# Optimization experiments

Hardware: AMD Instinct MI355X
Metric: run time of the kernel (lower is better)

Reference implementation:

```python
import jax, jax.numpy as jnp
import numpy as np

N_HEAD = 8
FACTOR = 5


def setup_inputs() -> dict:
    key = jax.random.key(0)
    ks = jax.random.split(key, 6)
    B, L, D = 2, 2048, 512
    sample_k = FACTOR * int(np.ceil(np.log(L)))  # 40
    std = float(np.sqrt(2.0 / (D + D)))
    x = jax.random.normal(ks[0], (B, L, D), jnp.float32)
    Wq = jax.random.normal(ks[1], (D, D), jnp.float32) * std
    Wk = jax.random.normal(ks[2], (D, D), jnp.float32) * std
    Wv = jax.random.normal(ks[3], (D, D), jnp.float32) * std
    bq = jnp.zeros((D,), jnp.float32)
    bk = jnp.zeros((D,), jnp.float32)
    bv = jnp.zeros((D,), jnp.float32)
    index_sample = jax.random.randint(ks[4], (L, sample_k), 0, L, dtype=jnp.int64)
    return {"x": x, "Wq": Wq, "bq": bq, "Wk": Wk, "bk": bk, "Wv": Wv, "bv": bv,
            "index_sample": index_sample}


def reference(x, Wq, bq, Wk, bk, Wv, bv, index_sample):
    B, L, D = x.shape
    H = N_HEAD
    dk = D // H
    u = min(FACTOR * int(np.ceil(np.log(L))), L)  # n_top == sample_k here

    def proj(W, b):
        # nn.Linear: x @ W.T + b, then split heads -> [B, H, L, dk]
        return (x @ W.T + b).reshape(B, L, H, dk).transpose(0, 2, 1, 3)

    q, k, v = proj(Wq, bq), proj(Wk, bk), proj(Wv, bv)

    # --- _prob_QK: sampled QK scores for query sparsity measure ---
    # K_sample[b,h,l,s,:] = k[b,h, index_sample[l,s], :]
    K_sample = k[:, :, index_sample]                      # [B,H,L,S,dk]
    Q_K_sample = jnp.einsum('bhld,bhlsd->bhls', q, K_sample)  # [B,H,L,S]
    M = Q_K_sample.max(-1) - Q_K_sample.sum(-1) / L       # sparsity measure [B,H,L]
    M_top = jax.lax.top_k(M, u)[1]                        # [B,H,u] top-query indices

    Q_reduce = jnp.take_along_axis(q, M_top[..., None], axis=2)  # [B,H,u,dk]
    scale = 1.0 / np.sqrt(dk)
    scores = jnp.einsum('bhud,bhld->bhul', Q_reduce, k) * scale  # [B,H,u,L]

    # --- initial context: causal cumulative sum of V (mask_flag=True) ---
    context = jnp.cumsum(v, axis=2)                       # [B,H,L,dk]

    # --- update context at the selected query rows ---
    attn = jax.nn.softmax(scores, axis=-1)                # [B,H,u,L]
    upd = jnp.einsum('bhul,bhld->bhud', attn, v)          # [B,H,u,dk]
    bidx = jnp.arange(B)[:, None, None]
    hidx = jnp.arange(H)[None, :, None]
    context = context.at[bidx, hidx, M_top].set(upd)

    attns = jnp.full((B, H, L, L), 1.0 / L, dtype=attn.dtype)
    attns = attns.at[bidx, hidx, M_top].set(attn)

    # NOTE: original reshapes [B,H,L,dk] -> [B,L,H*dk] WITHOUT transposing; keep faithful.
    return context.reshape(B, L, -1), attns
```

## Files before the change

### kernel.cpp

```cpp
#include <hip/hip_runtime.h>
#include <math.h>

#define BB 2
#define LL 2048
#define DD 512
#define HH 8
#define DK 64
#define SK 40
#define UU 40
#define BH (BB*HH)

typedef __attribute__((ext_vector_type(8))) __bf16 bf16x8;
typedef __attribute__((ext_vector_type(4))) float f32x4;

__device__ inline ushort f2bf_rn(float f) {
    unsigned u = __float_as_uint(f);
    unsigned r = (u + 0x7fffu + ((u >> 16) & 1u)) >> 16;
    return (ushort)r;
}
__device__ inline float bf2f(ushort h) { return __uint_as_float(((unsigned)h) << 16); }

__device__ __forceinline__ void gload16(const ushort* g, void* l) {
    __builtin_amdgcn_global_load_lds(
        (const __attribute__((address_space(1))) unsigned int*)g,
        (__attribute__((address_space(3))) unsigned int*)l,
        16, 0, 0);
}

__global__ __launch_bounds__(256) void pack_split(
    const float* __restrict__ x,
    const float* __restrict__ Wq, const float* __restrict__ Wk, const float* __restrict__ Wv,
    ushort* __restrict__ Ah, ushort* __restrict__ Al,
    ushort* __restrict__ Bh, ushort* __restrict__ Bl)
{
    const int bid = blockIdx.x;
    const float* src; ushort* dh; ushort* dl;
    if (bid < 1024) {
        const int g = bid * 256 + threadIdx.x;
        const int r = g >> 6, c = (g & 63) * 8;
        src = x + (long)r * DD + c;
        dh = Ah + (long)r * DD + c;
        dl = Al + (long)r * DD + c;
    } else {
        const int wb = bid - 1024;
        const int p = wb >> 7;
        const float* W = (p == 0) ? Wq : ((p == 1) ? Wk : Wv);
        const int rem = (wb & 127) * 256 + threadIdx.x;
        const int r = rem >> 6, c = (rem & 63) * 8;
        src = W + (long)r * DD + c;
        dh = Bh + ((long)p * DD + r) * DD + c;
        dl = Bl + ((long)p * DD + r) * DD + c;
    }
    const float4 f0 = *(const float4*)&src[0];
    const float4 f1 = *(const float4*)&src[4];
    float f[8] = {f0.x, f0.y, f0.z, f0.w, f1.x, f1.y, f1.z, f1.w};
    union { ushort s[8]; uint4 u; } H, L;
    #pragma unroll
    for (int i = 0; i < 8; ++i) {
        H.s[i] = f2bf_rn(f[i]);
        L.s[i] = f2bf_rn(f[i] - bf2f(H.s[i]));
    }
    *(uint4*)dh = H.u;
    *(uint4*)dl = L.u;
}

__global__ __launch_bounds__(256) void k1_proj_fill(
    const ushort* __restrict__ Ah, const ushort* __restrict__ Al,
    const ushort* __restrict__ Bh, const ushort* __restrict__ Bl,
    const float* __restrict__ bq, const float* __restrict__ bk_, const float* __restrict__ bv,
    float* __restrict__ q, float* __restrict__ k, float* __restrict__ v,
    float* __restrict__ attns)
{
    const int tid = threadIdx.x;

    if (blockIdx.x >= 384) {
        const float c = 1.0f / (float)LL;
        const float4 val = make_float4(c, c, c, c);
        float4* p = (float4*)attns + (long)(blockIdx.x - 384) * 8192 + tid;
        #pragma unroll
        for (int i = 0; i < 32; ++i) p[i * 256] = val;
        return;
    }

    const int pz = blockIdx.x >> 7;
    const int rem = blockIdx.x & 127;
    const int o0 = (rem >> 5) * 128;
    const int m0 = (rem & 31) * 128;
    const float* bias = (pz == 0) ? bq : ((pz == 1) ? bk_ : bv);
    float* out = (pz == 0) ? q : ((pz == 1) ? k : v);

    const ushort* Bp = Bh + (long)pz * DD * DD;
    const ushort* Blp = Bl + (long)pz * DD * DD;
    const ushort* segA[3] = {Ah, Ah, Al};
    const ushort* segB[3] = {Bp, Blp, Bp};

    __shared__ __attribute__((aligned(16))) ushort As[128 * 64];
    __shared__ __attribute__((aligned(16))) ushort Bs[128 * 64];

    const int lane = tid & 63, w = tid >> 6;
    const int wr = w >> 1, wc = w & 1;
    const int ln15 = lane & 15;
    const int l3 = lane >> 3, l7 = (lane & 7) * 8;

    f32x4 acc[4][4] = {};

    for (int t = 0; t < 24; ++t) {
        const ushort* Aseg = segA[t >> 3];
        const ushort* Bseg = segB[t >> 3];
        const int k0 = (t & 7) * 64;
        __syncthreads();
        #pragma unroll
        for (int c = 0; c < 8; ++c) {
            const int j = w * 8 + c;
            if (j < 16) {
                gload16(Aseg + (long)(m0 + j * 8 + l3) * DD + k0 + l7,
                        (char*)As + j * 1024);
            } else {
                const int j2 = j - 16;
                gload16(Bseg + (long)(o0 + j2 * 8 + l3) * DD + k0 + l7,
                        (char*)Bs + j2 * 1024);
            }
        }
        __syncthreads();
        #pragma unroll
        for (int ks = 0; ks < 2; ++ks) {
            const int kb = ks * 64 + (lane >> 4) * 16;
            bf16x8 bfr[4];
            #pragma unroll
            for (int jj = 0; jj < 4; ++jj)
                bfr[jj] = *(const bf16x8*)((const char*)Bs + (wc * 64 + jj * 16 + ln15) * 128 + kb);
            #pragma unroll
            for (int i = 0; i < 4; ++i) {
                bf16x8 af = *(const bf16x8*)((const char*)As + (wr * 64 + i * 16 + ln15) * 128 + kb);
                #pragma unroll
                for (int jj = 0; jj < 4; ++jj)
                    acc[i][jj] = __builtin_amdgcn_mfma_f32_16x16x32_bf16(af, bfr[jj], acc[i][jj], 0, 0, 0);
            }
        }
    }

    const int n_base = o0 + wc * 64;
    float bb[4];
    #pragma unroll
    for (int jj = 0; jj < 4; ++jj) bb[jj] = bias[n_base + jj * 16 + ln15];
    #pragma unroll
    for (int i = 0; i < 4; ++i) {
        #pragma unroll
        for (int jj = 0; jj < 4; ++jj) {
            const int n = n_base + jj * 16 + ln15;
            #pragma unroll
            for (int r = 0; r < 4; ++r) {
                const int m = m0 + wr * 64 + i * 16 + (lane >> 4) * 4 + r;
                out[(((long)(m >> 11) * HH + (n >> 6)) * LL + (m & (LL - 1))) * DK + (n & 63)] =
                    acc[i][jj][r] + bb[jj];
            }
        }
    }
}

__global__ __launch_bounds__(256) void k2_qk_cumsum1(
    const float* __restrict__ q, const float* __restrict__ k, const float* __restrict__ v,
    const int* __restrict__ idxs, float* __restrict__ M, float* __restrict__ sums)
{
    const int tid = threadIdx.x;

    if (blockIdx.x >= 512) {
        const int b = blockIdx.x - 512;
        const int bh = b >> 4;
        const int d = tid & 63, sc_ = tid >> 6;
        const int chunk = (b & 15) * 4 + sc_;
        const float* vb = v + ((long)bh * LL + chunk * 32) * DK + d;
        float s = 0.f;
        #pragma unroll
        for (int r = 0; r < 32; ++r) s += vb[r * DK];
        sums[((long)bh * 64 + chunk) * DK + d] = s;
        return;
    }

    const int g = blockIdx.x * 64 + (tid >> 2);
    const int part = tid & 3;
    const int bh = g >> 11, l = g & (LL - 1);
    const float* qr = q + ((long)bh * LL + l) * DK;
    float4 qv[16];
    #pragma unroll
    for (int i = 0; i < 16; ++i) qv[i] = *(const float4*)&qr[i * 4];

    const int* ir = idxs + (long)l * SK + part * 10;
    const float* kb = k + (long)bh * LL * DK;
    float mx = -INFINITY, sm = 0.f;
    #pragma unroll
    for (int s = 0; s < 10; ++s) {
        const float* kr = kb + (long)ir[s] * DK;
        float acc = 0.f;
        #pragma unroll
        for (int i = 0; i < 16; ++i) {
            float4 kv = *(const float4*)&kr[i * 4];
            acc += qv[i].x * kv.x + qv[i].y * kv.y + qv[i].z * kv.z + qv[i].w * kv.w;
        }
        mx = fmaxf(mx, acc); sm += acc;
    }
    mx = fmaxf(mx, __shfl_xor(mx, 1, 64));
    mx = fmaxf(mx, __shfl_xor(mx, 2, 64));
    sm += __shfl_xor(sm, 1, 64);
    sm += __shfl_xor(sm, 2, 64);
    if (part == 0) M[(long)bh * LL + l] = mx - sm * (1.0f / (float)LL);
}

__global__ __launch_bounds__(256) void k4_all(
    const float* __restrict__ q, const float* __restrict__ k, const float* __restrict__ v,
    const float* __restrict__ M, const float* __restrict__ sums,
    float* __restrict__ attns, float* __restrict__ ctx)
{
    const int tid = threadIdx.x;
    const bool isCum = blockIdx.x >= 128;
    const int bh = isCum ? ((blockIdx.x - 128) >> 4) : (blockIdx.x >> 3);

    __shared__ int list[UU];
    __shared__ unsigned bmap[64];

    if (tid < 64) bmap[tid] = 0u;
    __syncthreads();
    if (tid < 64) {
        const int lane = tid;
        float vals[32];
        #pragma unroll
        for (int r = 0; r < 32; ++r) vals[r] = M[(long)bh * LL + r * 64 + lane];
        for (int it = 0; it < UU; ++it) {
            float lm = vals[0];
            #pragma unroll
            for (int r = 1; r < 32; ++r) lm = fmaxf(lm, vals[r]);
            float wm = lm;
            #pragma unroll
            for (int s = 1; s < 64; s <<= 1) wm = fmaxf(wm, __shfl_xor(wm, s, 64));
            unsigned long long mask = __ballot(lm == wm);
            int first = (int)__ffsll(mask) - 1;
            if (lane == first) {
                #pragma unroll
                for (int r = 0; r < 32; ++r) {
                    if (vals[r] == wm) { list[it] = r * 64 + lane; vals[r] = -INFINITY; break; }
                }
            }
        }
    }
    __syncthreads();
    if (tid < UU) atomicOr(&bmap[list[tid] >> 5], 1u << (list[tid] & 31));
    __syncthreads();

    if (isCum) {
        const int b = blockIdx.x - 128;
        const int d = tid & 63, sc_ = tid >> 6;
        const int chunk = (b & 15) * 4 + sc_;
        float carry = 0.f;
        for (int c = 0; c < chunk; ++c) carry += sums[((long)bh * 64 + c) * DK + d];
        const float* vb = v + ((long)bh * LL + chunk * 32) * DK + d;
        float* cb = ctx + ((long)bh * LL + chunk * 32) * DK + d;
        float run = carry;
        #pragma unroll
        for (int r = 0; r < 32; ++r) {
            run += vb[r * DK];
            const int l = chunk * 32 + r;
            if (!((bmap[l >> 5] >> (l & 31)) & 1u)) cb[r * DK] = run;
        }
        return;
    }

    const int g = blockIdx.x & 7;
    const int lane = tid & 63, wave = tid >> 6;
    __shared__ float qs[5][DK];
    __shared__ float sc[5][LL];
    __shared__ float red[5][4];
    __shared__ float red2[4][5][DK];

    if (tid < 80) {
        int u = tid >> 4, c4 = (tid & 15) * 4;
        *(float4*)&qs[u][c4] = *(const float4*)&q[((long)bh * LL + list[g * 5 + u]) * DK + c4];
    }
    __syncthreads();

    const float* kb = k + (long)bh * LL * DK;
    float a[8][5] = {};
    #pragma unroll
    for (int c = 0; c < DK; c += 4) {
        float4 qv[5];
        #pragma unroll
        for (int u = 0; u < 5; ++u) qv[u] = *(const float4*)&qs[u][c];
        #pragma unroll
        for (int r = 0; r < 8; ++r) {
            float4 kv = *(const float4*)&kb[(long)(tid + r * 256) * DK + c];
            #pragma unroll
            for (int u = 0; u < 5; ++u)
                a[r][u] += qv[u].x * kv.x + qv[u].y * kv.y + qv[u].z * kv.z + qv[u].w * kv.w;
        }
    }
    const float scale = 0.125f;
    #pragma unroll
    for (int r = 0; r < 8; ++r)
        #pragma unroll
        for (int u = 0; u < 5; ++u)
            sc[u][tid + r * 256] = a[r][u] * scale;
    __syncthreads();

    float xv[5][8];
    #pragma unroll
    for (int u = 0; u < 5; ++u) {
        float4 t0 = *(const float4*)&sc[u][tid * 8];
        float4 t1 = *(const float4*)&sc[u][tid * 8 + 4];
        xv[u][0] = t0.x; xv[u][1] = t0.y; xv[u][2] = t0.z; xv[u][3] = t0.w;
        xv[u][4] = t1.x; xv[u][5] = t1.y; xv[u][6] = t1.z; xv[u][7] = t1.w;
    }
    float mloc[5];
    #pragma unroll
    for (int u = 0; u < 5; ++u) {
        float m = xv[u][0];
        #pragma unroll
        for (int i = 1; i < 8; ++i) m = fmaxf(m, xv[u][i]);
        #pragma unroll
        for (int s = 1; s < 64; s <<= 1) m = fmaxf(m, __shfl_xor(m, s, 64));
        if (lane == 0) red[u][wave] = m;
        mloc[u] = m;
    }
    __syncthreads();
    #pragma unroll
    for (int u = 0; u < 5; ++u)
        mloc[u] = fmaxf(fmaxf(red[u][0], red[u][1]), fmaxf(red[u][2], red[u][3]));
    __syncthreads();
    #pragma unroll
    for (int u = 0; u < 5; ++u) {
        float s = 0.f;
        #pragma unroll
        for (int i = 0; i < 8; ++i) { xv[u][i] = expf(xv[u][i] - mloc[u]); s += xv[u][i]; }
        #pragma unroll
        for (int st = 1; st < 64; st <<= 1) s += __shfl_xor(s, st, 64);
        if (lane == 0) red[u][wave] = s;
    }
    __syncthreads();
    #pragma unroll
    for (int u = 0; u < 5; ++u) {
        float inv = 1.0f / (red[u][0] + red[u][1] + red[u][2] + red[u][3]);
        float* row = attns + ((long)bh * LL + list[g * 5 + u]) * LL;
        float4 o0, o1;
        o0.x = xv[u][0] * inv; o0.y = xv[u][1] * inv; o0.z = xv[u][2] * inv; o0.w = xv[u][3] * inv;
        o1.x = xv[u][4] * inv; o1.y = xv[u][5] * inv; o1.z = xv[u][6] * inv; o1.w = xv[u][7] * inv;
        *(float4*)&row[tid * 8] = o0;
        *(float4*)&row[tid * 8 + 4] = o1;
        *(float4*)&sc[u][tid * 8] = o0;
        *(float4*)&sc[u][tid * 8 + 4] = o1;
    }
    __syncthreads();

    const int d = tid & 63, part = tid >> 6;
    const float* vb = v + (long)bh * LL * DK + d;
    float ua[5] = {};
    for (int l0 = part * 512; l0 < part * 512 + 512; l0 += 4) {
        float vv0 = vb[(long)(l0 + 0) * DK];
        float vv1 = vb[(long)(l0 + 1) * DK];
        float vv2 = vb[(long)(l0 + 2) * DK];
        float vv3 = vb[(long)(l0 + 3) * DK];
        #pragma unroll
        for (int u = 0; u < 5; ++u) {
            float4 pv = *(const float4*)&sc[u][l0];
            ua[u] += pv.x * vv0 + pv.y * vv1 + pv.z * vv2 + pv.w * vv3;
        }
    }
    #pragma unroll
    for (int u = 0; u < 5; ++u) red2[part][u][d] = ua[u];
    __syncthreads();
    if (part == 0) {
        #pragma unroll
        for (int u = 0; u < 5; ++u) {
            float s = red2[0][u][d] + red2[1][u][d] + red2[2][u][d] + red2[3][u][d];
            ctx[((long)bh * LL + list[g * 5 + u]) * DK + d] = s;
        }
    }
}

extern "C" void kernel_launch(void* const* d_in, const int* in_sizes, int n_in,
                              void* d_out, int out_size, void* d_ws, size_t ws_size,
                              hipStream_t stream) {
    const float* x  = (const float*)d_in[0];
    const float* Wq = (const float*)d_in[1];
    const float* bq = (const float*)d_in[2];
    const float* Wk = (const float*)d_in[3];
    const float* bk = (const float*)d_in[4];
    const float* Wv = (const float*)d_in[5];
    const float* bv = (const float*)d_in[6];
    const int* idxs = (const int*)d_in[7];

    float* ctx   = (float*)d_out;
    float* attns = (float*)d_out + (long)BB * HH * LL * DK;

    char* w = (char*)d_ws;
    float* q    = (float*)w; w += (size_t)BB * HH * LL * DK * 4;
    float* k    = (float*)w; w += (size_t)BB * HH * LL * DK * 4;
    float* v    = (float*)w; w += (size_t)BB * HH * LL * DK * 4;
    float* M    = (float*)w; w += (size_t)BB * HH * LL * 4;
    float* sums = (float*)w; w += (size_t)BH * 64 * DK * 4;
    ushort* Bh  = (ushort*)w; w += (size_t)3 * DD * DD * 2;
    ushort* Bl  = (ushort*)w; w += (size_t)3 * DD * DD * 2;

    ushort* Ah = (ushort*)ctx;
    ushort* Al = Ah + (size_t)4096 * DD;

    pack_split<<<1408, 256, 0, stream>>>(x, Wq, Wk, Wv, Ah, Al, Bh, Bl);

    k1_proj_fill<<<384 + 2048, 256, 0, stream>>>(Ah, Al, Bh, Bl, bq, bk, bv, q, k, v, attns);

    k2_qk_cumsum1<<<512 + 256, 256, 0, stream>>>(q, k, v, idxs, M, sums);

    k4_all<<<128 + 256, 256, 0, stream>>>(q, k, v, M, sums, attns, ctx);
}
```

Measured before the change: 226.5 us.

## Fuse all stages into one cooperative persistent kernel with grid syncs

Replaces the four separate launches (pack, projection plus fill, QK sampling plus chunk sums, top-k plus attention plus cumsum) with a single cooperative kernel of 512 persistent blocks separated by grid.sync barriers. The large constant fill of attns is now handed out in chunks through an atomic counter, so blocks that finish the projection GEMM pick up fill work. The aim is to remove inter-kernel launch gaps and tail idling. In exchange it adds three grid-wide barriers and keeps fewer blocks resident for the memory-bound fill. The original four-kernel path remains as a fallback if the cooperative launch fails.

```diff
diff --git a/kernel.cpp b/kernel.cpp
--- a/kernel.cpp
+++ b/kernel.cpp
@@ -1,5 +1,8 @@
 #include <hip/hip_runtime.h>
+#include <hip/hip_cooperative_groups.h>
 #include <math.h>
+
+namespace cg = cooperative_groups;
 
 #define BB 2
 #define LL 2048
@@ -9,6 +12,7 @@
 #define SK 40
 #define UU 40
 #define BH (BB*HH)
+#define NBLK 512
 
 typedef __attribute__((ext_vector_type(8))) __bf16 bf16x8;
 typedef __attribute__((ext_vector_type(4))) float f32x4;
@@ -25,6 +29,343 @@
         (const __attribute__((address_space(1))) unsigned int*)g,
         (__attribute__((address_space(3))) unsigned int*)l,
         16, 0, 0);
+}
+
+__global__ __launch_bounds__(256, 2) void mega(
+    const float* __restrict__ x,
+    const float* __restrict__ Wq, const float* __restrict__ Wk, const float* __restrict__ Wv,
+    const float* __restrict__ bq, const float* __restrict__ bk_, const float* __restrict__ bv,
+    const int* __restrict__ idxs,
+    float* __restrict__ q, float* __restrict__ k, float* __restrict__ v,
+    float* __restrict__ M, float* __restrict__ sums,
+    ushort* __restrict__ Ah, ushort* __restrict__ Al,
+    ushort* __restrict__ Bh, ushort* __restrict__ Bl,
+    float* __restrict__ ctx, float* __restrict__ attns,
+    unsigned* __restrict__ fillctr)
+{
+    cg::grid_group grid = cg::this_grid();
+    __shared__ __attribute__((aligned(16))) char smem[32768];
+    const int tid = threadIdx.x;
+    const int bid = blockIdx.x;
+
+    if (bid == 0 && tid == 0) *fillctr = 0u;
+    for (int vb = bid; vb < 1408; vb += NBLK) {
+        const float* src; ushort* dh; ushort* dl;
+        if (vb < 1024) {
+            const int g = vb * 256 + tid;
+            const int r = g >> 6, c = (g & 63) * 8;
+            src = x + (long)r * DD + c;
+            dh = Ah + (long)r * DD + c;
+            dl = Al + (long)r * DD + c;
+        } else {
+            const int wb = vb - 1024;
+            const int p = wb >> 7;
+            const float* W = (p == 0) ? Wq : ((p == 1) ? Wk : Wv);
+            const int rem = (wb & 127) * 256 + tid;
+            const int r = rem >> 6, c = (rem & 63) * 8;
+            src = W + (long)r * DD + c;
+            dh = Bh + ((long)p * DD + r) * DD + c;
+            dl = Bl + ((long)p * DD + r) * DD + c;
+        }
+        const float4 f0 = *(const float4*)&src[0];
+        const float4 f1 = *(const float4*)&src[4];
+        float f[8] = {f0.x, f0.y, f0.z, f0.w, f1.x, f1.y, f1.z, f1.w};
+        union { ushort s[8]; uint4 u; } H, L;
+        #pragma unroll
+        for (int i = 0; i < 8; ++i) {
+            H.s[i] = f2bf_rn(f[i]);
+            L.s[i] = f2bf_rn(f[i] - bf2f(H.s[i]));
+        }
+        *(uint4*)dh = H.u;
+        *(uint4*)dl = L.u;
+    }
+    grid.sync();
+
+    if (bid < 384) {
+        const int pz = bid >> 7;
+        const int rem = bid & 127;
+        const int o0 = (rem >> 5) * 128;
+        const int m0 = (rem & 31) * 128;
+        const float* bias = (pz == 0) ? bq : ((pz == 1) ? bk_ : bv);
+        float* out = (pz == 0) ? q : ((pz == 1) ? k : v);
+
+        const ushort* Bp = Bh + (long)pz * DD * DD;
+        const ushort* Blp = Bl + (long)pz * DD * DD;
+        const ushort* segA[3] = {Ah, Ah, Al};
+        const ushort* segB[3] = {Bp, Blp, Bp};
+
+        ushort* As = (ushort*)smem;
+        ushort* Bs = (ushort*)(smem + 16384);
+
+        const int lane = tid & 63, w = tid >> 6;
+        const int wr = w >> 1, wc = w & 1;
+        const int ln15 = lane & 15;
+        const int l3 = lane >> 3, l7 = (lane & 7) * 8;
+
+        f32x4 acc[4][4] = {};
+
+        for (int t = 0; t < 24; ++t) {
+            const ushort* Aseg = segA[t >> 3];
+            const ushort* Bseg = segB[t >> 3];
+            const int k0 = (t & 7) * 64;
+            __syncthreads();
+            #pragma unroll
+            for (int c = 0; c < 8; ++c) {
+                const int j = w * 8 + c;
+                if (j < 16) {
+                    gload16(Aseg + (long)(m0 + j * 8 + l3) * DD + k0 + l7,
+                            (char*)As + j * 1024);
+                } else {
+                    const int j2 = j - 16;
+                    gload16(Bseg + (long)(o0 + j2 * 8 + l3) * DD + k0 + l7,
+                            (char*)Bs + j2 * 1024);
+                }
+            }
+            __syncthreads();
+            #pragma unroll
+            for (int ks = 0; ks < 2; ++ks) {
+                const int kb = ks * 64 + (lane >> 4) * 16;
+                bf16x8 bfr[4];
+                #pragma unroll
+                for (int jj = 0; jj < 4; ++jj)
+                    bfr[jj] = *(const bf16x8*)((const char*)Bs + (wc * 64 + jj * 16 + ln15) * 128 + kb);
+                #pragma unroll
+                for (int i = 0; i < 4; ++i) {
+                    bf16x8 af = *(const bf16x8*)((const char*)As + (wr * 64 + i * 16 + ln15) * 128 + kb);
+                    #pragma unroll
+                    for (int jj = 0; jj < 4; ++jj)
+                        acc[i][jj] = __builtin_amdgcn_mfma_f32_16x16x32_bf16(af, bfr[jj], acc[i][jj], 0, 0, 0);
+                }
+            }
+        }
+
+        const int n_base = o0 + wc * 64;
+        float bb[4];
+        #pragma unroll
+        for (int jj = 0; jj < 4; ++jj) bb[jj] = bias[n_base + jj * 16 + ln15];
+        #pragma unroll
+        for (int i = 0; i < 4; ++i) {
+            #pragma unroll
+            for (int jj = 0; jj < 4; ++jj) {
+                const int n = n_base + jj * 16 + ln15;
+                #pragma unroll
+                for (int r = 0; r < 4; ++r) {
+                    const int m = m0 + wr * 64 + i * 16 + (lane >> 4) * 4 + r;
+                    out[(((long)(m >> 11) * HH + (n >> 6)) * LL + (m & (LL - 1))) * DK + (n & 63)] =
+                        acc[i][jj][r] + bb[jj];
+                }
+            }
+        }
+    }
+    {
+        volatile int* chunk_s = (volatile int*)smem;
+        const float c = 1.0f / (float)LL;
+        const float4 val = make_float4(c, c, c, c);
+        for (;;) {
+            __syncthreads();
+            if (tid == 0) *chunk_s = (int)atomicAdd(fillctr, 1u);
+            __syncthreads();
+            const int vb = *chunk_s;
+            if (vb >= 2048) break;
+            float4* p = (float4*)attns + (long)vb * 8192 + tid;
+            #pragma unroll
+            for (int i = 0; i < 32; ++i) p[i * 256] = val;
+        }
+    }
+    grid.sync();
+
+    {
+        const int g = bid * 64 + (tid >> 2);
+        const int part = tid & 3;
+        const int bh = g >> 11, l = g & (LL - 1);
+        const float* qr = q + ((long)bh * LL + l) * DK;
+        float4 qv[16];
+        #pragma unroll
+        for (int i = 0; i < 16; ++i) qv[i] = *(const float4*)&qr[i * 4];
+
+        const int* ir = idxs + (long)l * SK + part * 10;
+        const float* kb = k + (long)bh * LL * DK;
+        float mx = -INFINITY, sm = 0.f;
+        #pragma unroll
+        for (int s = 0; s < 10; ++s) {
+            const float* kr = kb + (long)ir[s] * DK;
+            float acc = 0.f;
+            #pragma unroll
+            for (int i = 0; i < 16; ++i) {
+                float4 kv = *(const float4*)&kr[i * 4];
+                acc += qv[i].x * kv.x + qv[i].y * kv.y + qv[i].z * kv.z + qv[i].w * kv.w;
+            }
+            mx = fmaxf(mx, acc); sm += acc;
+        }
+        mx = fmaxf(mx, __shfl_xor(mx, 1, 64));
+        mx = fmaxf(mx, __shfl_xor(mx, 2, 64));
+        sm += __shfl_xor(sm, 1, 64);
+        sm += __shfl_xor(sm, 2, 64);
+        if (part == 0) M[(long)bh * LL + l] = mx - sm * (1.0f / (float)LL);
+    }
+    if (bid < 256) {
+        const int bh = bid >> 4;
+        const int d = tid & 63, sc_ = tid >> 6;
+        const int chunk = (bid & 15) * 4 + sc_;
+        const float* vb = v + ((long)bh * LL + chunk * 32) * DK + d;
+        float s = 0.f;
+        #pragma unroll
+        for (int r = 0; r < 32; ++r) s += vb[r * DK];
+        sums[((long)bh * 64 + chunk) * DK + d] = s;
+    }
+    grid.sync();
+
+    if (bid >= 384) return;
+
+    const bool isCum = bid >= 128;
+    const int bh = isCum ? ((bid - 128) >> 4) : (bid >> 3);
+
+    int* list = (int*)smem;
+    unsigned* bmap = (unsigned*)(smem + 256);
+
+    if (tid < 64) bmap[tid] = 0u;
+    __syncthreads();
+    if (tid < 64) {
+        const int lane = tid;
+        float vals[32];
+        #pragma unroll
+        for (int r = 0; r < 32; ++r) vals[r] = M[(long)bh * LL + r * 64 + lane];
+        for (int it = 0; it < UU; ++it) {
+            float lm = vals[0];
+            #pragma unroll
+            for (int r = 1; r < 32; ++r) lm = fmaxf(lm, vals[r]);
+            float wm = lm;
+            #pragma unroll
+            for (int s = 1; s < 64; s <<= 1) wm = fmaxf(wm, __shfl_xor(wm, s, 64));
+            unsigned long long mask = __ballot(lm == wm);
+            int first = (int)__ffsll(mask) - 1;
+            if (lane == first) {
+                #pragma unroll
+                for (int r = 0; r < 32; ++r) {
+                    if (vals[r] == wm) { list[it] = r * 64 + lane; vals[r] = -INFINITY; break; }
+                }
+            }
+        }
+    }
+    __syncthreads();
+    if (tid < UU) atomicOr(&bmap[list[tid] >> 5], 1u << (list[tid] & 31));
+    __syncthreads();
+
+    if (isCum) {
+        const int b = bid - 128;
+        const int d = tid & 63, sc_ = tid >> 6;
+        const int chunk = (b & 15) * 4 + sc_;
+        float carry = 0.f;
+        for (int c = 0; c < chunk; ++c) carry += sums[((long)bh * 64 + c) * DK + d];
+        const float* vb = v + ((long)bh * LL + chunk * 32) * DK + d;
+        float* cb = ctx + ((long)bh * LL + chunk * 32) * DK + d;
+        float run = carry;
+        #pragma unroll
+        for (int r = 0; r < 32; ++r) {
+            run += vb[r * DK];
+            const int l = chunk * 32 + r;
+            if (!((bmap[l >> 5] >> (l & 31)) & 1u)) cb[r * DK] = run;
+        }
+        return;
+    }
+
+    const int g = bid & 7;
+    const int lane = tid & 63, wave = tid >> 6;
+    float (*qs)[DK]  = (float(*)[DK])(smem + 512);
+    float (*red)[4]  = (float(*)[4])(smem + 1792);
+    float (*red2)[5][DK] = (float(*)[5][DK])(smem + 2048);
+    ushort* scbf = (ushort*)(smem + 7168);
+
+    if (tid < 80) {
+        int u = tid >> 4, c4 = (tid & 15) * 4;
+        *(float4*)&qs[u][c4] = *(const float4*)&q[((long)bh * LL + list[g * 5 + u]) * DK + c4];
+    }
+    __syncthreads();
+
+    const float* kb = k + (long)bh * LL * DK;
+    float a[8][5] = {};
+    #pragma unroll
+    for (int c = 0; c < DK; c += 4) {
+        float4 qv[5];
+        #pragma unroll
+        for (int u = 0; u < 5; ++u) qv[u] = *(const float4*)&qs[u][c];
+        #pragma unroll
+        for (int r = 0; r < 8; ++r) {
+            float4 kv = *(const float4*)&kb[(long)(tid + r * 256) * DK + c];
+            #pragma unroll
+            for (int u = 0; u < 5; ++u)
+                a[r][u] += qv[u].x * kv.x + qv[u].y * kv.y + qv[u].z * kv.z + qv[u].w * kv.w;
+        }
+    }
+    const float scale = 0.125f;
+    #pragma unroll
+    for (int r = 0; r < 8; ++r)
+        #pragma unroll
+        for (int u = 0; u < 5; ++u)
+            a[r][u] *= scale;
+
+    float mloc[5];
+    #pragma unroll
+    for (int u = 0; u < 5; ++u) {
+        float m = a[0][u];
+        #pragma unroll
+        for (int r = 1; r < 8; ++r) m = fmaxf(m, a[r][u]);
+        #pragma unroll
+        for (int s = 1; s < 64; s <<= 1) m = fmaxf(m, __shfl_xor(m, s, 64));
+        if (lane == 0) red[u][wave] = m;
+    }
+    __syncthreads();
+    #pragma unroll
+    for (int u = 0; u < 5; ++u)
+        mloc[u] = fmaxf(fmaxf(red[u][0], red[u][1]), fmaxf(red[u][2], red[u][3]));
+    __syncthreads();
+    #pragma unroll
+    for (int u = 0; u < 5; ++u) {
+        float s = 0.f;
+        #pragma unroll
+        for (int r = 0; r < 8; ++r) { a[r][u] = expf(a[r][u] - mloc[u]); s += a[r][u]; }
+        #pragma unroll
+        for (int st = 1; st < 64; st <<= 1) s += __shfl_xor(s, st, 64);
+        if (lane == 0) red[u][wave] = s;
+    }
+    __syncthreads();
+    #pragma unroll
+    for (int u = 0; u < 5; ++u) {
+        const float inv = 1.0f / (red[u][0] + red[u][1] + red[u][2] + red[u][3]);
+        float* row = attns + ((long)bh * LL + list[g * 5 + u]) * LL;
+        #pragma unroll
+        for (int r = 0; r < 8; ++r) {
+            const float p = a[r][u] * inv;
+            row[tid + r * 256] = p;
+            scbf[u * LL + tid + r * 256] = f2bf_rn(p);
+        }
+    }
+    __syncthreads();
+
+    const int d = tid & 63, part = tid >> 6;
+    const float* vb = v + (long)bh * LL * DK + d;
+    float ua[5] = {};
+    for (int l0 = part * 512; l0 < part * 512 + 512; l0 += 4) {
+        float vv0 = vb[(long)(l0 + 0) * DK];
+        float vv1 = vb[(long)(l0 + 1) * DK];
+        float vv2 = vb[(long)(l0 + 2) * DK];
+        float vv3 = vb[(long)(l0 + 3) * DK];
+        #pragma unroll
+        for (int u = 0; u < 5; ++u) {
+            ushort4 pv = *(const ushort4*)&scbf[u * LL + l0];
+            ua[u] += bf2f(pv.x) * vv0 + bf2f(pv.y) * vv1 + bf2f(pv.z) * vv2 + bf2f(pv.w) * vv3;
+        }
+    }
+    #pragma unroll
+    for (int u = 0; u < 5; ++u) red2[part][u][d] = ua[u];
+    __syncthreads();
+    if (part == 0) {
+        #pragma unroll
+        for (int u = 0; u < 5; ++u) {
+            float s = red2[0][u][d] + red2[1][u][d] + red2[2][u][d] + red2[3][u][d];
+            ctx[((long)bh * LL + list[g * 5 + u]) * DK + d] = s;
+        }
+    }
 }
 
 __global__ __launch_bounds__(256) void pack_split(
@@ -397,15 +738,24 @@
     float* sums = (float*)w; w += (size_t)BH * 64 * DK * 4;
     ushort* Bh  = (ushort*)w; w += (size_t)3 * DD * DD * 2;
     ushort* Bl  = (ushort*)w; w += (size_t)3 * DD * DD * 2;
+    unsigned* fillctr = (unsigned*)w; w += 256;
 
     ushort* Ah = (ushort*)ctx;
     ushort* Al = Ah + (size_t)4096 * DD;
 
-    pack_split<<<1408, 256, 0, stream>>>(x, Wq, Wk, Wv, Ah, Al, Bh, Bl);
-
-    k1_proj_fill<<<384 + 2048, 256, 0, stream>>>(Ah, Al, Bh, Bl, bq, bk, bv, q, k, v, attns);
-
-    k2_qk_cumsum1<<<512 + 256, 256, 0, stream>>>(q, k, v, idxs, M, sums);
-
-    k4_all<<<128 + 256, 256, 0, stream>>>(q, k, v, M, sums, attns, ctx);
+    void* args[] = {
+        (void*)&x, (void*)&Wq, (void*)&Wk, (void*)&Wv,
+        (void*)&bq, (void*)&bk, (void*)&bv, (void*)&idxs,
+        (void*)&q, (void*)&k, (void*)&v, (void*)&M, (void*)&sums,
+        (void*)&Ah, (void*)&Al, (void*)&Bh, (void*)&Bl,
+        (void*)&ctx, (void*)&attns, (void*)&fillctr
+    };
+    hipError_t err = hipLaunchCooperativeKernel((const void*)mega, dim3(NBLK), dim3(256),
+                                                args, 0, stream);
+    if (err != hipSuccess) {
+        pack_split<<<1408, 256, 0, stream>>>(x, Wq, Wk, Wv, Ah, Al, Bh, Bl);
+        k1_proj_fill<<<384 + 2048, 256, 0, stream>>>(Ah, Al, Bh, Bl, bq, bk, bv, q, k, v, attns);
+        k2_qk_cumsum1<<<512 + 256, 256, 0, stream>>>(q, k, v, idxs, M, sums);
+        k4_all<<<128 + 256, 256, 0, stream>>>(q, k, v, M, sums, attns, ctx);
+    }
 }
```

Result: slower. 630.1 us (+178.2%).
